# Kernel optimization log

Hardware: AMD Instinct MI355X
Metric: run time of the kernel (lower is better)

Reference implementation:

```python
import jax, jax.numpy as jnp
import numpy as np

B, N, D, H = 8, 1024, 1024, 16
HEAD_DIM = D // H
SCALING = HEAD_DIM ** (-0.5)
NEG = -1000000000.0


def setup_inputs() -> dict:
    key = jax.random.key(0)
    ks = jax.random.split(key, 7)
    x = jax.random.normal(ks[0], (B, N, D), dtype=jnp.float32)
    # variable-length batch: lengths in [N//2, N], mask[b, i] = i < len_b
    lengths = jax.random.randint(ks[1], (B,), N // 2, N + 1)
    mask = jnp.arange(N)[None, :] < lengths[:, None]  # [B, N] bool
    s = D ** (-0.5)
    Wk = jax.random.normal(ks[2], (D, D), dtype=jnp.float32) * s
    Wq = jax.random.normal(ks[3], (D, D), dtype=jnp.float32) * s
    Wv = jax.random.normal(ks[4], (D, D), dtype=jnp.float32) * s
    Wo = jax.random.normal(ks[5], (D, D), dtype=jnp.float32) * s
    bo = jnp.zeros((D,), dtype=jnp.float32)
    return {"x": x, "mask": mask, "Wk": Wk, "Wq": Wq, "Wv": Wv, "Wo": Wo, "bo": bo}


def reference(x, mask, Wk, Wq, Wv, Wo, bo):
    # torch nn.Linear: y = x @ W.T
    keys = (x @ Wk.T).reshape(B, N, H, HEAD_DIM)
    queries = (x @ Wq.T).reshape(B, N, H, HEAD_DIM)
    values = (x @ Wv.T).reshape(B, N, H, HEAD_DIM)
    # NOTE: faithful to source: keys on i, queries on j, softmax over j
    scores = jnp.einsum('bihx,bjhx->bhij', keys, queries) * SCALING  # [B,H,N,N]
    pair_mask = mask[:, None, :] & mask[:, :, None]                  # [B,N,N]
    scores = scores + jnp.where(pair_mask, 0.0, NEG)[:, None, :, :]
    attn = jax.nn.softmax(scores, axis=-1)
    out = jnp.einsum('bhij,bjhx->bihx', attn, values)                # [B,N,H,hd]
    out = out.reshape(B, N, D)
    out = out @ Wo.T + bo
    # source does out_dense[mask] (ragged); static-shape equivalent: zero padding
    return out * mask[:, :, None].astype(out.dtype)
```

## Files before the change

### kernel.cpp

```cpp
#include <hip/hip_runtime.h>

typedef unsigned short u16;
typedef __attribute__((ext_vector_type(8))) short short8;
typedef __attribute__((ext_vector_type(4))) short short4v;
typedef __attribute__((ext_vector_type(4))) float f32x4;
typedef __attribute__((ext_vector_type(16))) float f32x16;

#define MFMA16(a, b, c) __builtin_amdgcn_mfma_f32_16x16x32_bf16(a, b, c, 0, 0, 0)
#define MFMA32(a, b, c) __builtin_amdgcn_mfma_f32_32x32x16_bf16(a, b, c, 0, 0, 0)

#define BB 8
#define NN 1024
#define DD 1024
#define HH 16
#define HD 64
#define MM (BB * NN)
#define SCLOG2 0.18033688011112042f

static __device__ __forceinline__ u16 f2bf(float f) {
  unsigned u = __float_as_uint(f);
  u += 0x7fffu + ((u >> 16) & 1u);
  return (u16)(u >> 16);
}

static __device__ __forceinline__ void gld16(const void* g, void* l) {
  __builtin_amdgcn_global_load_lds((const __attribute__((address_space(1))) void*)g,
                                   (__attribute__((address_space(3))) void*)l, 16, 0, 0);
}

static __device__ __forceinline__ unsigned cvtpk(float lo, float hi) {
  unsigned r;
  asm("v_cvt_pk_bf16_f32 %0, %1, %2" : "=v"(r) : "v"(lo), "v"(hi));
  return r;
}

static __device__ __forceinline__ f32x16 zero16() {
  f32x16 v;
#pragma unroll
  for (int i = 0; i < 16; ++i) v[i] = 0.f;
  return v;
}

__global__ void lens_kernel(const unsigned char* __restrict__ mask, int* __restrict__ lens) {
  __shared__ int acc[BB];
  const int t = threadIdx.x;
  if (t < BB) acc[t] = 0;
  __syncthreads();
  const bool isbyte = (mask[1] != 0);
  for (int b = 0; b < BB; ++b) {
    int s = 0;
    if (isbyte) {
      for (int i = t; i < NN; i += 256) s += mask[(size_t)b * NN + i] ? 1 : 0;
    } else {
      const int* mi = (const int*)mask;
      for (int i = t; i < NN; i += 256) s += mi[(size_t)b * NN + i] != 0 ? 1 : 0;
    }
    if (s) atomicAdd(&acc[b], s);
  }
  __syncthreads();
  if (t < BB) lens[t] = acc[t];
}

__global__ __launch_bounds__(256) void cast_bf16_kernel(const float* __restrict__ in,
                                                        u16* __restrict__ out, int n8) {
  const int i = blockIdx.x * 256 + threadIdx.x;
  if (i >= n8) return;
  const f32x4* p = (const f32x4*)in + (size_t)i * 2;
  const f32x4 a = p[0], b = p[1];
  short8 o;
  o[0] = (short)f2bf(a[0]); o[1] = (short)f2bf(a[1]);
  o[2] = (short)f2bf(a[2]); o[3] = (short)f2bf(a[3]);
  o[4] = (short)f2bf(b[0]); o[5] = (short)f2bf(b[1]);
  o[6] = (short)f2bf(b[2]); o[7] = (short)f2bf(b[3]);
  *(short8*)(out + (size_t)i * 8) = o;
}

__global__ __launch_bounds__(256) void cast4_bf16_kernel(const float* __restrict__ a, const float* __restrict__ b,
                                                         const float* __restrict__ c, const float* __restrict__ d,
                                                         u16* __restrict__ oa, u16* __restrict__ ob,
                                                         u16* __restrict__ oc, u16* __restrict__ od) {
  const int i = blockIdx.x * 256 + threadIdx.x;
  const float* in;
  u16* out;
  switch (blockIdx.y) {
    case 0: in = a; out = oa; break;
    case 1: in = b; out = ob; break;
    case 2: in = c; out = oc; break;
    default: in = d; out = od; break;
  }
  const f32x4* p = (const f32x4*)in + (size_t)i * 2;
  const f32x4 va = p[0], vb = p[1];
  short8 o;
  o[0] = (short)f2bf(va[0]); o[1] = (short)f2bf(va[1]);
  o[2] = (short)f2bf(va[2]); o[3] = (short)f2bf(va[3]);
  o[4] = (short)f2bf(vb[0]); o[5] = (short)f2bf(vb[1]);
  o[6] = (short)f2bf(vb[2]); o[7] = (short)f2bf(vb[3]);
  *(short8*)(out + (size_t)i * 8) = o;
}

#define GEMM_CORE(A_, B_)                                                       \
  for (int k0 = 0; k0 < 1024; k0 += 64) {                                       \
    __syncthreads();                                                            \
    _Pragma("unroll") for (int p = 0; p < 4; ++p) {                             \
      const int off = (p * 256 + t) * 16;                                       \
      const int row = off >> 7;                                                 \
      const int colb = (off & 127) ^ ((row & 7) << 4);                          \
      gld16(A_ + (size_t)(m0 + row) * 1024 + k0 + (colb >> 1), As + off / 2);   \
      gld16(B_ + (size_t)(n0 + row) * 1024 + k0 + (colb >> 1), Bs + off / 2);   \
    }                                                                           \
    __syncthreads();                                                            \
    _Pragma("unroll") for (int ks = 0; ks < 2; ++ks) {                          \
      short8 af[4], bf[4];                                                      \
      _Pragma("unroll") for (int mi = 0; mi < 4; ++mi) {                        \
        const int row = wr * 64 + mi * 16 + li;                                 \
        const int byo = row * 128 + ((ks * 64 + lg * 16) ^ ((row & 7) << 4));   \
        af[mi] = *(const short8*)((const char*)As + byo);                       \
      }                                                                         \
      _Pragma("unroll") for (int ni = 0; ni < 4; ++ni) {                        \
        const int row = wc * 64 + ni * 16 + li;                                 \
        const int byo = row * 128 + ((ks * 64 + lg * 16) ^ ((row & 7) << 4));   \
        bf[ni] = *(const short8*)((const char*)Bs + byo);                       \
      }                                                                         \
      __builtin_amdgcn_s_setprio(1);                                            \
      _Pragma("unroll") for (int mi = 0; mi < 4; ++mi)                          \
        _Pragma("unroll") for (int ni = 0; ni < 4; ++ni)                        \
            acc[mi][ni] = MFMA16(af[mi], bf[ni], acc[mi][ni]);                  \
      __builtin_amdgcn_s_setprio(0);                                            \
    }                                                                           \
  }

__global__ __launch_bounds__(256) void gemm_qkv(const u16* __restrict__ A,
                                                const u16* __restrict__ Wk3, const u16* __restrict__ Wq3,
                                                const u16* __restrict__ Wv3,
                                                u16* __restrict__ kb, u16* __restrict__ qb,
                                                u16* __restrict__ vtb, const int* __restrict__ lens) {
  const int m0 = blockIdx.x * 128;
  if ((m0 & 1023) >= lens[m0 >> 10]) return;
  __shared__ u16 As[128 * 64];
  __shared__ u16 Bs[128 * 64];
  const int mat = blockIdx.y >> 3;
  const int n0 = (blockIdx.y & 7) * 128;
  const u16* Bw = (mat == 0) ? Wk3 : (mat == 1) ? Wq3 : Wv3;
  const int t = threadIdx.x;
  const int lane = t & 63;
  const int w = t >> 6;
  const int wr = w >> 1, wc = w & 1;
  const int li = lane & 15, lg = lane >> 4;
  f32x4 acc[4][4] = {};

  GEMM_CORE(A, Bw)

  if (mat == 2) {
#pragma unroll
    for (int mi = 0; mi < 4; ++mi) {
      const int row = m0 + wr * 64 + mi * 16 + lg * 4;
      const int bb = row >> 10, jj = row & 1023;
#pragma unroll
      for (int ni = 0; ni < 4; ++ni) {
        const int col = n0 + wc * 64 + ni * 16 + li;
        const int h = col >> 6, x = col & 63;
        short4v st;
#pragma unroll
        for (int r = 0; r < 4; ++r) st[r] = (short)f2bf(acc[mi][ni][r]);
        *(short4v*)(vtb + ((size_t)((bb * HH + h) * HD + x)) * NN + jj) = st;
      }
    }
  } else {
    u16* C = (mat == 0) ? kb : qb;
    const float scale = (mat == 0) ? SCLOG2 : 1.0f;
#pragma unroll
    for (int mi = 0; mi < 4; ++mi)
#pragma unroll
      for (int ni = 0; ni < 4; ++ni) {
        const int col = n0 + wc * 64 + ni * 16 + li;
        const int rowb = m0 + wr * 64 + mi * 16 + lg * 4;
#pragma unroll
        for (int r = 0; r < 4; ++r)
          C[(size_t)(rowb + r) * 1024 + col] = f2bf(acc[mi][ni][r] * scale);
      }
  }
}

__global__ __launch_bounds__(256) void gemm_out(const u16* __restrict__ A, const u16* __restrict__ Bw,
                                                float* __restrict__ C, const float* __restrict__ bias,
                                                const int* __restrict__ lens) {
  const int m0 = blockIdx.x * 128;
  const int n0 = blockIdx.y * 128;
  const int t = threadIdx.x;
  if ((m0 & 1023) >= lens[m0 >> 10]) {
    const int r = t >> 1, ch = (t & 1) * 64;
    float* Crow = C + (size_t)(m0 + r) * 1024 + n0 + ch;
    const f32x4 z = {0.f, 0.f, 0.f, 0.f};
#pragma unroll
    for (int c = 0; c < 16; ++c) *(f32x4*)(Crow + c * 4) = z;
    return;
  }
  __shared__ u16 As[128 * 64];
  __shared__ u16 Bs[128 * 64];
  const int lane = t & 63;
  const int w = t >> 6;
  const int wr = w >> 1, wc = w & 1;
  const int li = lane & 15, lg = lane >> 4;
  f32x4 acc[4][4] = {};

  GEMM_CORE(A, Bw)

#pragma unroll
  for (int ni = 0; ni < 4; ++ni) {
    const int col = n0 + wc * 64 + ni * 16 + li;
    const float bv = bias[col];
#pragma unroll
    for (int mi = 0; mi < 4; ++mi) {
      const int rowb = m0 + wr * 64 + mi * 16 + lg * 4;
#pragma unroll
      for (int r = 0; r < 4; ++r) {
        const int row = rowb + r;
        const int bb = row >> 10, ii = row & 1023;
        const float v = (ii < lens[bb]) ? (acc[mi][ni][r] + bv) : 0.f;
        C[(size_t)row * 1024 + col] = v;
      }
    }
  }
}

__global__ __launch_bounds__(256) void attn_kernel(const u16* __restrict__ Kb, const u16* __restrict__ Qb,
                                                   const u16* __restrict__ Vtb, u16* __restrict__ attb,
                                                   const int* __restrict__ lens) {
  const int bid = blockIdx.x;
  const int b = bid >> 7;
  const int ic = (bid >> 3) & 7;
  const int h = ((bid & 7) << 1) | ((bid >> 6) & 1);
  const int len = lens[b];
  const int i0 = ic * 128;
  if (i0 >= len) return;
  const int t = threadIdx.x;
  const int w = t >> 6, l = t & 63;
  const int l31 = l & 31, hi = l >> 5;
  const int i0w = i0 + w * 32;

  __shared__ u16 Qs[2][4096];
  __shared__ u16 Vs[2][4096];

  short8 kf[4];
  {
    const u16* kp = Kb + ((size_t)(b * NN + i0w + l31)) * DD + h * HD + hi * 8;
#pragma unroll
    for (int ks = 0; ks < 4; ++ks) kf[ks] = *(const short8*)(kp + ks * 16);
  }

  const size_t qsrc = ((size_t)(b * NN) + l31) * DD + h * HD + w * 16 + hi * 8;
  const size_t vsrc = ((size_t)((b * HH + h) * HD + l31)) * NN + w * 16 + hi * 8;

  auto STAGE = [&](int buf, int j0) {
    u16* qd = &Qs[buf][0] + t * 8;
    u16* vd = &Vs[buf][0] + t * 8;
    gld16(Qb + qsrc + (size_t)j0 * DD, qd);
    gld16(Qb + qsrc + (size_t)(j0 + 32) * DD, qd + 2048);
    gld16(Vtb + vsrc + j0, vd);
    gld16(Vtb + vsrc + 32 * NN + j0, vd + 2048);
  };

  f32x16 o0 = zero16(), o1 = zero16();
  float m_run = -3.0e38f, l_run = 0.f;
  const int nt = (len + 63) >> 6;

  STAGE(0, 0);
  __syncthreads();
  for (int jt = 0; jt < nt; ++jt) {
    const int cur = jt & 1;
    const int j0 = jt * 64;
    if (jt + 1 < nt) STAGE(cur ^ 1, j0 + 64);

    const u16* Qc = &Qs[cur][0];
    const u16* Vc = &Vs[cur][0];
    f32x16 s0 = zero16(), s1 = zero16();
    __builtin_amdgcn_s_setprio(1);
#pragma unroll
    for (int ks = 0; ks < 4; ++ks) {
      const short8 qf = *(const short8*)(Qc + (ks * 64 + l) * 8);
      s0 = MFMA32(qf, kf[ks], s0);
    }
#pragma unroll
    for (int ks = 0; ks < 4; ++ks) {
      const short8 qf = *(const short8*)(Qc + ((4 + ks) * 64 + l) * 8);
      s1 = MFMA32(qf, kf[ks], s1);
    }
    __builtin_amdgcn_s_setprio(0);

    if (j0 + 64 > len) {
#pragma unroll
      for (int r = 0; r < 16; ++r) {
        const int jl = (r & 3) + 8 * (r >> 2) + 4 * hi;
        if (j0 + jl >= len) s0[r] = -3.0e38f;
        if (j0 + 32 + jl >= len) s1[r] = -3.0e38f;
      }
    }

    float pmax = s0[0];
#pragma unroll
    for (int r = 1; r < 16; ++r) pmax = fmaxf(pmax, s0[r]);
#pragma unroll
    for (int r = 0; r < 16; ++r) pmax = fmaxf(pmax, s1[r]);
    pmax = fmaxf(pmax, __shfl_xor(pmax, 32));

    if (!__all(pmax <= m_run + 11.5f)) {
      const float mnew = fmaxf(m_run, pmax);
      const float al = __builtin_amdgcn_exp2f(m_run - mnew);
      l_run *= al;
#pragma unroll
      for (int r = 0; r < 16; ++r) { o0[r] *= al; o1[r] *= al; }
      m_run = mnew;
    }

    float rs = 0.f;
#pragma unroll
    for (int r = 0; r < 16; ++r) { const float p = __builtin_amdgcn_exp2f(s0[r] - m_run); s0[r] = p; rs += p; }
#pragma unroll
    for (int r = 0; r < 16; ++r) { const float p = __builtin_amdgcn_exp2f(s1[r] - m_run); s1[r] = p; rs += p; }
    rs += __shfl_xor(rs, 32);
    l_run += rs;

    short8 pf[4];
#pragma unroll
    for (int jk = 0; jk < 4; ++jk) {
      const f32x16& ss = (jk < 2) ? s0 : s1;
      const int kk = jk & 1;
      unsigned W0 = cvtpk(ss[8 * kk + 0], ss[8 * kk + 1]);
      unsigned W1 = cvtpk(ss[8 * kk + 2], ss[8 * kk + 3]);
      unsigned W2 = cvtpk(ss[8 * kk + 4], ss[8 * kk + 5]);
      unsigned W3 = cvtpk(ss[8 * kk + 6], ss[8 * kk + 7]);
      asm("v_permlane32_swap_b32 %0, %1" : "+v"(W0), "+v"(W2));
      asm("v_permlane32_swap_b32 %0, %1" : "+v"(W1), "+v"(W3));
      union { unsigned u[4]; short8 s; } pu;
      pu.u[0] = W0; pu.u[1] = W1; pu.u[2] = W2; pu.u[3] = W3;
      pf[jk] = pu.s;
    }

    __builtin_amdgcn_s_setprio(1);
#pragma unroll
    for (int kkg = 0; kkg < 4; ++kkg) {
      const short8 vf = *(const short8*)(Vc + (kkg * 64 + l) * 8);
      o0 = MFMA32(vf, pf[kkg], o0);
    }
#pragma unroll
    for (int kkg = 0; kkg < 4; ++kkg) {
      const short8 vf = *(const short8*)(Vc + ((4 + kkg) * 64 + l) * 8);
      o1 = MFMA32(vf, pf[kkg], o1);
    }
    __builtin_amdgcn_s_setprio(0);
    __syncthreads();
  }

  const float inv = 1.f / l_run;
  u16* op = attb + (size_t)(b * NN + i0w + l31) * DD + h * HD + hi * 4;
#pragma unroll
  for (int xs = 0; xs < 2; ++xs) {
    const f32x16& oo = xs ? o1 : o0;
#pragma unroll
    for (int q = 0; q < 4; ++q) {
      short4v st;
#pragma unroll
      for (int e = 0; e < 4; ++e) st[e] = (short)f2bf(oo[q * 4 + e] * inv);
      *(short4v*)(op + xs * 32 + q * 8) = st;
    }
  }
}

extern "C" void kernel_launch(void* const* d_in, const int* in_sizes, int n_in,
                              void* d_out, int out_size, void* d_ws, size_t ws_size,
                              hipStream_t stream) {
  const float* x = (const float*)d_in[0];
  const unsigned char* mask = (const unsigned char*)d_in[1];
  const float* Wk = (const float*)d_in[2];
  const float* Wq = (const float*)d_in[3];
  const float* Wv = (const float*)d_in[4];
  const float* Wo = (const float*)d_in[5];
  const float* bo = (const float*)d_in[6];
  float* out = (float*)d_out;

  char* ws = (char*)d_ws;
  size_t o = 0;
  int* lens = (int*)(ws + o); o += 256;
  u16* xb  = (u16*)(ws + o); o += (size_t)MM * DD * 2;
  u16* wkb = (u16*)(ws + o); o += (size_t)DD * DD * 2;
  u16* wqb = (u16*)(ws + o); o += (size_t)DD * DD * 2;
  u16* wvb = (u16*)(ws + o); o += (size_t)DD * DD * 2;
  u16* wob = (u16*)(ws + o); o += (size_t)DD * DD * 2;
  u16* kb  = (u16*)(ws + o); o += (size_t)MM * DD * 2;
  u16* qb  = (u16*)(ws + o); o += (size_t)MM * DD * 2;
  u16* vtb = (u16*)(ws + o); o += (size_t)MM * DD * 2;
  u16* attb = xb;

  lens_kernel<<<dim3(1), dim3(256), 0, stream>>>(mask, lens);

  const int xn8 = MM * DD / 8;
  cast_bf16_kernel<<<dim3(xn8 / 256), dim3(256), 0, stream>>>(x, xb, xn8);
  cast4_bf16_kernel<<<dim3(DD * DD / 8 / 256, 4), dim3(256), 0, stream>>>(
      Wk, Wq, Wv, Wo, wkb, wqb, wvb, wob);

  gemm_qkv<<<dim3(MM / 128, 24), dim3(256), 0, stream>>>(xb, wkb, wqb, wvb, kb, qb, vtb, lens);

  attn_kernel<<<dim3(1024), dim3(256), 0, stream>>>(kb, qb, vtb, attb, lens);

  gemm_out<<<dim3(MM / 128, DD / 128), dim3(256), 0, stream>>>(attb, wob, out, bo, lens);
}
```

Before: 186.4 us.

## Double-buffer LDS tiles in projection GEMMs with BK=32 prefetch

Replaces the single-buffered 128x128x64 GEMM main loop, used by the QKV and output projection kernels, with a double-buffered BK=32 loop. The next tile's global-to-LDS load is issued before computing on the current tile, and the swizzle is adjusted to the 64-byte row. The aim is to overlap global loads with MFMA work and cut the load/compute barrier pair per iteration down to one. In exchange there are twice as many iterations with half the MFMA work each, so per-iteration overhead and barrier count relative to compute go up.

```diff
diff --git a/kernel.cpp b/kernel.cpp
--- a/kernel.cpp
+++ b/kernel.cpp
@@ -98,35 +98,38 @@
   *(short8*)(out + (size_t)i * 8) = o;
 }
 
-#define GEMM_CORE(A_, B_)                                                       \
-  for (int k0 = 0; k0 < 1024; k0 += 64) {                                       \
+#define STAGE_G(d, k0_)                                                            \
+  _Pragma("unroll") for (int p = 0; p < 2; ++p) {                                  \
+    const int off = (p * 256 + t) * 16;                                            \
+    const int row = off >> 6;                                                      \
+    const int colb = (off & 63) ^ ((row & 3) << 4);                                \
+    gld16(Ag + (size_t)(m0 + row) * 1024 + (k0_) + (colb >> 1), &As[d][off >> 1]); \
+    gld16(Bg + (size_t)(n0 + row) * 1024 + (k0_) + (colb >> 1), &Bs[d][off >> 1]); \
+  }
+
+#define GEMM_CORE2()                                                            \
+  STAGE_G(0, 0)                                                                 \
+  __syncthreads();                                                              \
+  for (int k0 = 0; k0 < 1024; k0 += 32) {                                       \
+    const int cur = (k0 >> 5) & 1;                                              \
+    if (k0 + 32 < 1024) { STAGE_G(cur ^ 1, k0 + 32) }                           \
+    short8 af[4], bf[4];                                                        \
+    _Pragma("unroll") for (int mi = 0; mi < 4; ++mi) {                          \
+      const int row = wr * 64 + mi * 16 + li;                                   \
+      const int byo = row * 64 + ((lg * 16) ^ ((row & 3) << 4));                \
+      af[mi] = *(const short8*)((const char*)&As[cur][0] + byo);                \
+    }                                                                           \
+    _Pragma("unroll") for (int ni = 0; ni < 4; ++ni) {                          \
+      const int row = wc * 64 + ni * 16 + li;                                   \
+      const int byo = row * 64 + ((lg * 16) ^ ((row & 3) << 4));                \
+      bf[ni] = *(const short8*)((const char*)&Bs[cur][0] + byo);                \
+    }                                                                           \
+    __builtin_amdgcn_s_setprio(1);                                              \
+    _Pragma("unroll") for (int mi = 0; mi < 4; ++mi)                            \
+      _Pragma("unroll") for (int ni = 0; ni < 4; ++ni)                          \
+          acc[mi][ni] = MFMA16(af[mi], bf[ni], acc[mi][ni]);                    \
+    __builtin_amdgcn_s_setprio(0);                                              \
     __syncthreads();                                                            \
-    _Pragma("unroll") for (int p = 0; p < 4; ++p) {                             \
-      const int off = (p * 256 + t) * 16;                                       \
-      const int row = off >> 7;                                                 \
-      const int colb = (off & 127) ^ ((row & 7) << 4);                          \
-      gld16(A_ + (size_t)(m0 + row) * 1024 + k0 + (colb >> 1), As + off / 2);   \
-      gld16(B_ + (size_t)(n0 + row) * 1024 + k0 + (colb >> 1), Bs + off / 2);   \
-    }                                                                           \
-    __syncthreads();                                                            \
-    _Pragma("unroll") for (int ks = 0; ks < 2; ++ks) {                          \
-      short8 af[4], bf[4];                                                      \
-      _Pragma("unroll") for (int mi = 0; mi < 4; ++mi) {                        \
-        const int row = wr * 64 + mi * 16 + li;                                 \
-        const int byo = row * 128 + ((ks * 64 + lg * 16) ^ ((row & 7) << 4));   \
-        af[mi] = *(const short8*)((const char*)As + byo);                       \
-      }                                                                         \
-      _Pragma("unroll") for (int ni = 0; ni < 4; ++ni) {                        \
-        const int row = wc * 64 + ni * 16 + li;                                 \
-        const int byo = row * 128 + ((ks * 64 + lg * 16) ^ ((row & 7) << 4));   \
-        bf[ni] = *(const short8*)((const char*)Bs + byo);                       \
-      }                                                                         \
-      __builtin_amdgcn_s_setprio(1);                                            \
-      _Pragma("unroll") for (int mi = 0; mi < 4; ++mi)                          \
-        _Pragma("unroll") for (int ni = 0; ni < 4; ++ni)                        \
-            acc[mi][ni] = MFMA16(af[mi], bf[ni], acc[mi][ni]);                  \
-      __builtin_amdgcn_s_setprio(0);                                            \
-    }                                                                           \
   }
 
 __global__ __launch_bounds__(256) void gemm_qkv(const u16* __restrict__ A,
@@ -136,11 +139,12 @@
                                                 u16* __restrict__ vtb, const int* __restrict__ lens) {
   const int m0 = blockIdx.x * 128;
   if ((m0 & 1023) >= lens[m0 >> 10]) return;
-  __shared__ u16 As[128 * 64];
-  __shared__ u16 Bs[128 * 64];
+  __shared__ u16 As[2][4096];
+  __shared__ u16 Bs[2][4096];
   const int mat = blockIdx.y >> 3;
   const int n0 = (blockIdx.y & 7) * 128;
-  const u16* Bw = (mat == 0) ? Wk3 : (mat == 1) ? Wq3 : Wv3;
+  const u16* Ag = A;
+  const u16* Bg = (mat == 0) ? Wk3 : (mat == 1) ? Wq3 : Wv3;
   const int t = threadIdx.x;
   const int lane = t & 63;
   const int w = t >> 6;
@@ -148,7 +152,7 @@
   const int li = lane & 15, lg = lane >> 4;
   f32x4 acc[4][4] = {};
 
-  GEMM_CORE(A, Bw)
+  GEMM_CORE2()
 
   if (mat == 2) {
 #pragma unroll
@@ -195,15 +199,17 @@
     for (int c = 0; c < 16; ++c) *(f32x4*)(Crow + c * 4) = z;
     return;
   }
-  __shared__ u16 As[128 * 64];
-  __shared__ u16 Bs[128 * 64];
+  __shared__ u16 As[2][4096];
+  __shared__ u16 Bs[2][4096];
+  const u16* Ag = A;
+  const u16* Bg = Bw;
   const int lane = t & 63;
   const int w = t >> 6;
   const int wr = w >> 1, wc = w & 1;
   const int li = lane & 15, lg = lane >> 4;
   f32x4 acc[4][4] = {};
 
-  GEMM_CORE(A, Bw)
+  GEMM_CORE2()
 
 #pragma unroll
   for (int ni = 0; ni < 4; ++ni) {
```

New measurement: 187.1 us. Within noise of the previous version (+0.4%).
